# Kernel optimization log

Hardware: AMD Instinct MI355X
Metric: run time of the kernel (lower is better)

The kernel has to match this reference:

```python
import jax, jax.numpy as jnp
import numpy as np

KS = 3          # kernel_size
DIL = 6         # dilation
PAD = 6         # padding
N = KS * KS     # sampling points per pixel
EPS = 1e-5      # BatchNorm eps


def conv2d(x, w, b=None, padding=0):
    out = jax.lax.conv_general_dilated(
        x, w, window_strides=(1, 1),
        padding=[(padding, padding), (padding, padding)],
        dimension_numbers=('NCHW', 'OIHW', 'NCHW'))
    if b is not None:
        out = out + b[None, :, None, None]
    return out


def setup_inputs() -> dict:
    key = jax.random.key(0)
    ks = jax.random.split(key, 6)
    B, C, H, W, P = 4, 256, 64, 64, 256
    x = jax.random.normal(ks[0], (B, C, H, W), jnp.float32)
    # offset-predicting conv (2N channels), kaiming-ish scale, kept small so offsets are sane
    w_p = jax.random.normal(ks[1], (2 * N, C, 3, 3), jnp.float32) * 0.02
    b_p = jnp.zeros((2 * N,), jnp.float32)
    # modulation-mask conv (N channels)
    w_m = jax.random.normal(ks[2], (N, C, 3, 3), jnp.float32) * 0.02
    b_m = jnp.zeros((N,), jnp.float32)
    # main deform-conv weight (no bias)
    w = jax.random.normal(ks[3], (P, C, KS, KS), jnp.float32) * (2.0 / (C * N)) ** 0.5
    gamma = jnp.ones((P,), jnp.float32)   # BN weight (init fill 1)
    beta = jnp.zeros((P,), jnp.float32)   # BN bias  (init fill 0)
    return dict(x=x, w_p=w_p, b_p=b_p, w_m=w_m, b_m=b_m, w=w, gamma=gamma, beta=beta)


def deform_conv(x, w_p, b_p, w_m, b_m, w):
    B, C, H, W = x.shape
    offset = conv2d(x, w_p, b_p, padding=1)                 # [B, 2N, H, W]
    m = jax.nn.sigmoid(conv2d(x, w_m, b_m, padding=1))      # [B, N, H, W] modulation mask

    x_pad = jnp.pad(x, ((0, 0), (0, 0), (PAD, PAD), (PAD, PAD)))
    Hp, Wp = H + 2 * PAD, W + 2 * PAD

    # p = p_0 (base grid, starts at 1 into padded map) + p_n (dilated kernel grid) + offset
    r = (KS - 1) // 2
    pn = jnp.arange(-r, r + 1, dtype=jnp.float32) * DIL
    pn_x, pn_y = jnp.meshgrid(pn, pn, indexing='ij')        # row-major matches conv weight layout
    p0_x = jnp.arange(1, H + 1, dtype=jnp.float32)
    p0_y = jnp.arange(1, W + 1, dtype=jnp.float32)
    off_x = offset[:, :N].transpose(0, 2, 3, 1)             # [B, H, W, N]
    off_y = offset[:, N:].transpose(0, 2, 3, 1)
    px = p0_x[None, :, None, None] + pn_x.reshape(-1)[None, None, None, :] + off_x
    py = p0_y[None, None, :, None] + pn_y.reshape(-1)[None, None, None, :] + off_y

    q_lt_x = jnp.clip(jnp.floor(px), 0, Hp - 1)
    q_lt_y = jnp.clip(jnp.floor(py), 0, Wp - 1)
    q_rb_x = jnp.clip(jnp.floor(px) + 1, 0, Hp - 1)
    q_rb_y = jnp.clip(jnp.floor(py) + 1, 0, Wp - 1)
    px = jnp.clip(px, 0, Hp - 1)
    py = jnp.clip(py, 0, Wp - 1)

    x_flat = x_pad.reshape(B, C, Hp * Wp)

    def gather(qx, qy):
        idx = (qx * Wp + qy).astype(jnp.int32).reshape(B, 1, -1)   # [B,1,H*W*N]
        v = jnp.take_along_axis(x_flat, jnp.broadcast_to(idx, (B, C, idx.shape[-1])), axis=2)
        return v.reshape(B, C, H, W, N)

    # bilinear weights (deform-conv-v2 formulation)
    g_lt = (1 + (q_lt_x - px)) * (1 + (q_lt_y - py))
    g_rb = (1 - (q_rb_x - px)) * (1 - (q_rb_y - py))
    g_lb = (1 + (q_lt_x - px)) * (1 - (q_rb_y - py))
    g_rt = (1 - (q_rb_x - px)) * (1 + (q_lt_y - py))

    x_off = (g_lt[:, None] * gather(q_lt_x, q_lt_y)
             + g_rb[:, None] * gather(q_rb_x, q_rb_y)
             + g_lb[:, None] * gather(q_lt_x, q_rb_y)
             + g_rt[:, None] * gather(q_rb_x, q_lt_y))     # [B, C, H, W, N]

    x_off = x_off * m.transpose(0, 2, 3, 1)[:, None]        # apply modulation

    # stride-KS conv over the tiled x_offset == einsum over kernel positions
    wk = w.reshape(w.shape[0], C, N)
    return jnp.einsum('bchwk,ock->bohw', x_off, wk)


def reference(x, w_p, b_p, w_m, b_m, w, gamma, beta):
    y = deform_conv(x, w_p, b_p, w_m, b_m, w)
    # BatchNorm2d, training mode (batch stats, biased variance)
    mean = y.mean(axis=(0, 2, 3), keepdims=True)
    var = ((y - mean) ** 2).mean(axis=(0, 2, 3), keepdims=True)
    y = (y - mean) * jax.lax.rsqrt(var + EPS)
    y = y * gamma[None, :, None, None] + beta[None, :, None, None]
    return jax.nn.relu(y)
```

## Files before the change

### kernel.cpp

```cpp
#include <hip/hip_runtime.h>
#include <math.h>

#define CC 256
#define PP 256
#define XSTR 296

#define WS_OFF   0ull
#define WS_Y     442368ull
#define WS_SUM   4636672ull
#define WS_SUMSQ 4636928ull
#define WS_SCALE 4637184ull
#define WS_SHIFT 4637440ull
#define WS_XT    4637696ull
#define WS_WF    8832000ull
#define WS_WPMF  9126912ull

typedef __attribute__((ext_vector_type(8))) short bf16x8;
typedef __attribute__((ext_vector_type(4))) float f32x4;

static __device__ inline unsigned short f2bf(float f) {
  unsigned int u = __float_as_uint(f);
  unsigned int r = (u + 0x7FFFu + ((u >> 16) & 1u)) >> 16;
  return (unsigned short)r;
}

__global__ __launch_bounds__(256) void k_prep(const float* __restrict__ x,
                                              const float* __restrict__ w,
                                              const float* __restrict__ w_p,
                                              const float* __restrict__ w_m,
                                              float* __restrict__ ws) {
  int blk = blockIdx.x, t = threadIdx.x;
  if (blk < 1024) {
    __shared__ float sT[64][65];
    int b = blk >> 8, h = (blk >> 2) & 63, c0 = (blk & 3) * 64;
    const float* xs = x + ((size_t)(b * 256 + c0) * 64 + h) * 64;
    int cl = t >> 6, wl = t & 63;
#pragma unroll
    for (int it = 0; it < 16; ++it) {
      int c = cl + it * 4;
      sT[c][wl] = xs[(size_t)c * 4096 + wl];
    }
    __syncthreads();
    float* xt = ws + WS_XT + ((size_t)b * 64 + h) * 16384 + c0;
    int c2 = t & 63, w2l = t >> 6;
#pragma unroll
    for (int it = 0; it < 16; ++it) {
      int w2 = w2l + it * 4;
      xt[(size_t)w2 * 256 + c2] = sT[c2][w2];
    }
  } else {
    int gid = (blk - 1024) * 256 + t;
    if (blk == 1024 && t < 512) ws[WS_SUM + t] = 0.f;
    unsigned short* wfb = (unsigned short*)(ws + WS_WF);
    for (int e = gid; e < 589824; e += 163840) {
      int j = e & 7, ocin = (e >> 3) & 15, quad = (e >> 7) & 3;
      int ot = (e >> 9) & 15, ksg = e >> 13;
      int kb = ksg / 9, ks = ksg - kb * 9;
      int c = kb * 32 + quad * 8 + j;
      int oc = ot * 16 + ocin;
      wfb[e] = f2bf(w[((size_t)oc * CC + c) * 9 + ks]);
    }
    unsigned short* wpmf = (unsigned short*)(ws + WS_WPMF);
    for (int e = gid; e < 73728; e += 163840) {
      int j = e & 7, ocin = (e >> 3) & 15, quad = (e >> 7) & 3;
      int ot = (e >> 9) & 1, ksg = e >> 10;
      int kb = ksg / 9, ks = ksg - kb * 9;
      int c = kb * 32 + quad * 8 + j;
      int oc = ot * 16 + ocin;
      float v = 0.f;
      if (oc < 18)      v = w_p[((size_t)oc * CC + c) * 9 + ks];
      else if (oc < 27) v = w_m[((size_t)(oc - 18) * CC + c) * 9 + ks];
      wpmf[e] = f2bf(v);
    }
  }
}

__global__ __launch_bounds__(512, 4) void k_offmask(const float* __restrict__ b_p,
                                                    const float* __restrict__ b_m,
                                                    float* __restrict__ ws) {
  const float* xT = ws + WS_XT;
  const unsigned short* wpmf = (const unsigned short*)(ws + WS_WPMF);
  float* offm = ws + WS_OFF;
  __shared__ __align__(16) unsigned short sXo0[32 * XSTR];
  __shared__ __align__(16) unsigned short sXo1[32 * XSTR];

  int t = threadIdx.x, blk = blockIdx.x;
  int xcd = blk & 7, ii = blk >> 3;
  int b = xcd >> 1, h = (xcd & 1) * 32 + (ii >> 1), side = ii & 1;

  int lane = t & 63, wv = __builtin_amdgcn_readfirstlane(t >> 6);
  int pxt = wv & 1, ot = (wv >> 1) & 1, kh = wv >> 2;
  f32x4 acc = {0.f, 0.f, 0.f, 0.f};
  const float4* xb4 = (const float4*)(xT + (size_t)b * 1048576);
  int uq = t >> 3, q = t & 7;

  int oa[5], odst[5];
#pragma unroll
  for (int r = 0; r < 5; ++r) {
    int u = r * 64 + uq;
    if (u < 288) {
      int j = u >> 5, px = u & 31;
      int row = h + j / 3 - 1, col = side * 32 + px + j % 3 - 1;
      odst[r] = px * XSTR + j * 32 + q * 4;
      oa[r] = ((unsigned)row < 64u && (unsigned)col < 64u)
                  ? (row * 64 + col) * 64 + q : -1;
    } else {
      odst[r] = -1;
      oa[r] = -1;
    }
  }

  auto stage = [&](int kb, unsigned short* buf) {
    int cb = kb * 8;
#pragma unroll
    for (int r = 0; r < 5; ++r) {
      if (odst[r] >= 0) {
        float4 v = {0.f, 0.f, 0.f, 0.f};
        if (oa[r] >= 0) v = xb4[oa[r] + cb];
        unsigned p0 = (unsigned)f2bf(v.x) | ((unsigned)f2bf(v.y) << 16);
        unsigned p1 = (unsigned)f2bf(v.z) | ((unsigned)f2bf(v.w) << 16);
        *(uint2*)&buf[odst[r]] = (uint2){p0, p1};
      }
    }
  };

  stage(0, sXo0);
  __syncthreads();
  for (int kb = 0; kb < 8; ++kb) {
    unsigned short* cur = (kb & 1) ? sXo1 : sXo0;
    unsigned short* nxt = (kb & 1) ? sXo0 : sXo1;
    if (kb < 7) stage(kb + 1, nxt);
    const unsigned short* bb =
        &cur[(pxt * 16 + (lane & 15)) * XSTR + (lane >> 4) * 8];
#pragma unroll
    for (int ks = 0; ks < 9; ++ks) {
      if ((int)(ks >= 5) == kh) {
        int ksg = kb * 9 + ks;
        bf16x8 af =
            *(const bf16x8*)(wpmf + (size_t)ksg * 1024 + ot * 512 + lane * 8);
        bf16x8 bf = *(const bf16x8*)(bb + ks * 32);
        acc = __builtin_amdgcn_mfma_f32_16x16x32_bf16(af, bf, acc, 0, 0, 0);
      }
    }
    __syncthreads();
  }

  float* sR = (float*)sXo0;
  if (kh == 1) {
    int base = (pxt * 2 + ot) * 256 + lane * 4;
#pragma unroll
    for (int r = 0; r < 4; ++r) sR[base + r] = acc[r];
  }
  __syncthreads();
  if (kh == 0) {
    int base = (pxt * 2 + ot) * 256 + lane * 4;
    int pxl = side * 32 + pxt * 16 + (lane & 15);
#pragma unroll
    for (int r = 0; r < 4; ++r) {
      int oc = ot * 16 + (lane >> 4) * 4 + r;
      if (oc < 27) {
        float v = acc[r] + sR[base + r];
        v += (oc < 18) ? b_p[oc] : b_m[oc - 18];
        if (oc >= 18) v = 1.f / (1.f + expf(-v));
        offm[((size_t)b * 27 + oc) * 4096 + h * 64 + pxl] = v;
      }
    }
  }
}

__global__ __launch_bounds__(512, 4) void k_deform(float* __restrict__ ws) {
  const float* offm = ws + WS_OFF;
  const float* xT = ws + WS_XT;
  const unsigned short* wfb = (const unsigned short*)(ws + WS_WF);
  float* y = ws + WS_Y;

  __shared__ __align__(16) uint4 sPK[288];
  __shared__ __align__(16) unsigned short sXu0[32 * XSTR];
  __shared__ __align__(16) unsigned short sXu1[32 * XSTR];

  int t = threadIdx.x, blk = blockIdx.x;
  int xcd = blk & 7, ii = blk >> 3;
  int b = xcd >> 1, h = (xcd & 1) * 32 + (ii >> 1), side = ii & 1;

  if (t < 288) {
    int k = t >> 5, w = side * 32 + (t & 31);
    size_t base = ((size_t)b * 27) * 4096 + h * 64 + w;
    float offx = offm[base + (size_t)k * 4096];
    float offy = offm[base + (size_t)(9 + k) * 4096];
    float mk   = offm[base + (size_t)(18 + k) * 4096];
    float pnx = (float)((k / 3 - 1) * 6);
    float pny = (float)((k % 3 - 1) * 6);
    float pxf = (float)(h + 1) + pnx + offx;
    float pyf = (float)(w + 1) + pny + offy;
    float fx = floorf(pxf), fy = floorf(pyf);
    float q0x = fminf(fmaxf(fx, 0.f), 75.f);
    float q1x = fminf(fmaxf(fx + 1.f, 0.f), 75.f);
    float q0y = fminf(fmaxf(fy, 0.f), 75.f);
    float q1y = fminf(fmaxf(fy + 1.f, 0.f), 75.f);
    float pxc = fminf(fmaxf(pxf, 0.f), 75.f);
    float pyc = fminf(fmaxf(pyf, 0.f), 75.f);
    float glt = (1.f + (q0x - pxc)) * (1.f + (q0y - pyc));
    float grb = (1.f - (q1x - pxc)) * (1.f - (q1y - pyc));
    float glb = (1.f + (q0x - pxc)) * (1.f - (q1y - pyc));
    float grt = (1.f - (q1x - pxc)) * (1.f + (q0y - pyc));
    int ix0 = (int)q0x - 6, ix1 = (int)q1x - 6;
    int iy0 = (int)q0y - 6, iy1 = (int)q1y - 6;
    bool v00 = (unsigned)ix0 < 64u && (unsigned)iy0 < 64u;
    bool v11 = (unsigned)ix1 < 64u && (unsigned)iy1 < 64u;
    bool v01 = (unsigned)ix0 < 64u && (unsigned)iy1 < 64u;
    bool v10 = (unsigned)ix1 < 64u && (unsigned)iy0 < 64u;
    unsigned a0 = v00 ? (unsigned)(ix0 * 64 + iy0) : 0u;
    unsigned a1 = v11 ? (unsigned)(ix1 * 64 + iy1) : 0u;
    unsigned a2 = v01 ? (unsigned)(ix0 * 64 + iy1) : 0u;
    unsigned a3 = v10 ? (unsigned)(ix1 * 64 + iy0) : 0u;
    float g0 = v00 ? glt * mk : 0.f;
    float g1 = v11 ? grb * mk : 0.f;
    float g2 = v01 ? glb * mk : 0.f;
    float g3 = v10 ? grt * mk : 0.f;
    uint4 pk;
    pk.x = a0 | (a1 << 16);
    pk.y = a2 | (a3 << 16);
    pk.z = (unsigned)f2bf(g0) | ((unsigned)f2bf(g1) << 16);
    pk.w = (unsigned)f2bf(g2) | ((unsigned)f2bf(g3) << 16);
    sPK[t] = pk;
  }
  __syncthreads();

  int uq = t >> 3, q = t & 7;
  int ta0[5], ta1[5], ta2[5], ta3[5], tdst[5];
  float tg0[5], tg1[5], tg2[5], tg3[5];
#pragma unroll
  for (int r = 0; r < 5; ++r) {
    int u = r * 64 + uq;
    if (u < 288) {
      uint4 pk = sPK[u];
      int k = u >> 5, px = u & 31;
      ta0[r] = (int)(pk.x & 0xFFFFu) * 64 + q;
      ta1[r] = (int)(pk.x >> 16) * 64 + q;
      ta2[r] = (int)(pk.y & 0xFFFFu) * 64 + q;
      ta3[r] = (int)(pk.y >> 16) * 64 + q;
      tg0[r] = __uint_as_float((pk.z & 0xFFFFu) << 16);
      tg1[r] = __uint_as_float(pk.z & 0xFFFF0000u);
      tg2[r] = __uint_as_float((pk.w & 0xFFFFu) << 16);
      tg3[r] = __uint_as_float(pk.w & 0xFFFF0000u);
      tdst[r] = px * XSTR + k * 32 + q * 4;
    } else {
      tdst[r] = -1;
    }
  }

  int lane = t & 63, wv = __builtin_amdgcn_readfirstlane(t >> 6);
  f32x4 acc[2][2];
#pragma unroll
  for (int i = 0; i < 2; ++i)
#pragma unroll
    for (int jj = 0; jj < 2; ++jj) acc[i][jj] = (f32x4){0.f, 0.f, 0.f, 0.f};

  const float4* xb4 = (const float4*)(xT + (size_t)b * 1048576);

  auto stage = [&](int kb, unsigned short* buf) {
    int cb = kb * 8;
#pragma unroll
    for (int r = 0; r < 5; ++r) {
      if (tdst[r] >= 0) {
        float4 v0 = xb4[ta0[r] + cb];
        float4 v1 = xb4[ta1[r] + cb];
        float4 v2 = xb4[ta2[r] + cb];
        float4 v3 = xb4[ta3[r] + cb];
        float g0 = tg0[r], g1 = tg1[r], g2 = tg2[r], g3 = tg3[r];
        float4 val;
        val.x = fmaf(g3, v3.x, fmaf(g2, v2.x, fmaf(g1, v1.x, g0 * v0.x)));
        val.y = fmaf(g3, v3.y, fmaf(g2, v2.y, fmaf(g1, v1.y, g0 * v0.y)));
        val.z = fmaf(g3, v3.z, fmaf(g2, v2.z, fmaf(g1, v1.z, g0 * v0.z)));
        val.w = fmaf(g3, v3.w, fmaf(g2, v2.w, fmaf(g1, v1.w, g0 * v0.w)));
        unsigned p0 = (unsigned)f2bf(val.x) | ((unsigned)f2bf(val.y) << 16);
        unsigned p1 = (unsigned)f2bf(val.z) | ((unsigned)f2bf(val.w) << 16);
        *(uint2*)&buf[tdst[r]] = (uint2){p0, p1};
      }
    }
  };

  stage(0, sXu0);
  __syncthreads();
  for (int kb = 0; kb < 8; ++kb) {
    unsigned short* cur = (kb & 1) ? sXu1 : sXu0;
    unsigned short* nxt = (kb & 1) ? sXu0 : sXu1;
    if (kb < 7) stage(kb + 1, nxt);
    const unsigned short* bb0 = &cur[(lane & 15) * XSTR + (lane >> 4) * 8];
    const unsigned short* bb1 = bb0 + 16 * XSTR;
#pragma unroll
    for (int ks = 0; ks < 9; ++ks) {
      int ksg = kb * 9 + ks;
      const unsigned short* ap =
          wfb + (size_t)ksg * 8192 + (size_t)wv * 1024 + lane * 8;
      bf16x8 af0 = *(const bf16x8*)ap;
      bf16x8 af1 = *(const bf16x8*)(ap + 512);
      bf16x8 bf0 = *(const bf16x8*)(bb0 + ks * 32);
      bf16x8 bf1 = *(const bf16x8*)(bb1 + ks * 32);
      acc[0][0] = __builtin_amdgcn_mfma_f32_16x16x32_bf16(af0, bf0, acc[0][0], 0, 0, 0);
      acc[0][1] = __builtin_amdgcn_mfma_f32_16x16x32_bf16(af0, bf1, acc[0][1], 0, 0, 0);
      acc[1][0] = __builtin_amdgcn_mfma_f32_16x16x32_bf16(af1, bf0, acc[1][0], 0, 0, 0);
      acc[1][1] = __builtin_amdgcn_mfma_f32_16x16x32_bf16(af1, bf1, acc[1][1], 0, 0, 0);
    }
    __syncthreads();
  }

  float* sP = (float*)sPK;
  float* sP2 = sP + 256;
  int quad = lane >> 4, li = lane & 15;
  size_t ybase = ((size_t)b * PP) * 4096 + h * 64 + side * 32;
#pragma unroll
  for (int otl = 0; otl < 2; ++otl) {
#pragma unroll
    for (int r = 0; r < 4; ++r) {
      int oc = wv * 32 + otl * 16 + quad * 4 + r;
      float v0 = acc[otl][0][r];
      float v1 = acc[otl][1][r];
      float* yp = y + ybase + (size_t)oc * 4096 + li;
      yp[0] = v0;
      yp[16] = v1;
      float s = v0 + v1;
      float s2 = fmaf(v0, v0, v1 * v1);
      s += __shfl_xor(s, 1);  s2 += __shfl_xor(s2, 1);
      s += __shfl_xor(s, 2);  s2 += __shfl_xor(s2, 2);
      s += __shfl_xor(s, 4);  s2 += __shfl_xor(s2, 4);
      s += __shfl_xor(s, 8);  s2 += __shfl_xor(s2, 8);
      if (li == 0) {
        sP[oc] = s;
        sP2[oc] = s2;
      }
    }
  }
  __syncthreads();
  if (t < 256) {
    atomicAdd(&ws[WS_SUM + t], sP[t]);
    atomicAdd(&ws[WS_SUMSQ + t], sP2[t]);
  }
}

__global__ void k_stats(float* __restrict__ ws, const float* __restrict__ gamma,
                        const float* __restrict__ beta) {
  int t = threadIdx.x;
  float s  = ws[WS_SUM + t];
  float s2 = ws[WS_SUMSQ + t];
  float mean = s * (1.f / 16384.f);
  float var  = fmaf(s2, 1.f / 16384.f, -mean * mean);
  float rstd = rsqrtf(var + 1e-5f);
  float sc = gamma[t] * rstd;
  ws[WS_SCALE + t] = sc;
  ws[WS_SHIFT + t] = fmaf(-mean, sc, beta[t]);
}

__global__ void k_bnrelu(const float* __restrict__ ws, float* __restrict__ out) {
  const float4* y4 = (const float4*)(ws + WS_Y);
  const float* scale = ws + WS_SCALE;
  const float* shift = ws + WS_SHIFT;
  float4* o4 = (float4*)out;
  const int n4 = 4 * PP * 1024;
  for (int i = blockIdx.x * blockDim.x + threadIdx.x; i < n4;
       i += gridDim.x * blockDim.x) {
    int oc = (i >> 10) & 255;
    float sc = scale[oc], sh = shift[oc];
    float4 v = y4[i];
    float4 r;
    r.x = fmaxf(fmaf(v.x, sc, sh), 0.f);
    r.y = fmaxf(fmaf(v.y, sc, sh), 0.f);
    r.z = fmaxf(fmaf(v.z, sc, sh), 0.f);
    r.w = fmaxf(fmaf(v.w, sc, sh), 0.f);
    o4[i] = r;
  }
}

extern "C" void kernel_launch(void* const* d_in, const int* in_sizes, int n_in,
                              void* d_out, int out_size, void* d_ws,
                              size_t ws_size, hipStream_t stream) {
  const float* x     = (const float*)d_in[0];
  const float* w_p   = (const float*)d_in[1];
  const float* b_p   = (const float*)d_in[2];
  const float* w_m   = (const float*)d_in[3];
  const float* b_m   = (const float*)d_in[4];
  const float* w     = (const float*)d_in[5];
  const float* gamma = (const float*)d_in[6];
  const float* beta  = (const float*)d_in[7];
  float* ws  = (float*)d_ws;
  float* out = (float*)d_out;

  k_prep<<<1664, 256, 0, stream>>>(x, w, w_p, w_m, ws);
  k_offmask<<<512, 512, 0, stream>>>(b_p, b_m, ws);
  k_deform<<<512, 512, 0, stream>>>(ws);
  k_stats<<<1, 256, 0, stream>>>(ws, gamma, beta);
  k_bnrelu<<<2048, 256, 0, stream>>>(ws, out);
}
```

Baseline: 167.9 us.

## Store transposed input as bf16 and gather 8-channel vectors in deform/offset kernels

The prep kernel now writes the channel-last copy of x as bf16 instead of fp32, halving the workspace footprint and the gather traffic in both the offset/mask conv and the deformable sampling kernel. Each thread now loads 16-byte bf16x8 vectors covering 8 channels, and the thread-to-sample mapping changes from 8 to 4 threads per sample. The deform kernel drops the shared-memory packing stage and its barrier, so each thread computes its own bilinear addresses and weights redundantly. The scratch for the epilogue reuses a staging buffer. The cost is that input values are rounded to bf16 before bilinear interpolation rather than after, which adds an extra rounding step.

```diff
diff --git a/kernel.cpp b/kernel.cpp
--- a/kernel.cpp
+++ b/kernel.cpp
@@ -12,8 +12,8 @@
 #define WS_SCALE 4637184ull
 #define WS_SHIFT 4637440ull
 #define WS_XT    4637696ull
-#define WS_WF    8832000ull
-#define WS_WPMF  9126912ull
+#define WS_WF    6734848ull
+#define WS_WPMF  7029760ull
 
 typedef __attribute__((ext_vector_type(8))) short bf16x8;
 typedef __attribute__((ext_vector_type(4))) float f32x4;
@@ -22,6 +22,9 @@
   unsigned int u = __float_as_uint(f);
   unsigned int r = (u + 0x7FFFu + ((u >> 16) & 1u)) >> 16;
   return (unsigned short)r;
+}
+static __device__ inline float bf2f(short s) {
+  return __uint_as_float(((unsigned)(unsigned short)s) << 16);
 }
 
 __global__ __launch_bounds__(256) void k_prep(const float* __restrict__ x,
@@ -41,12 +44,13 @@
       sT[c][wl] = xs[(size_t)c * 4096 + wl];
     }
     __syncthreads();
-    float* xt = ws + WS_XT + ((size_t)b * 64 + h) * 16384 + c0;
+    unsigned short* xt = (unsigned short*)(ws + WS_XT) +
+                         ((size_t)b * 64 + h) * 16384 + c0;
     int c2 = t & 63, w2l = t >> 6;
 #pragma unroll
     for (int it = 0; it < 16; ++it) {
       int w2 = w2l + it * 4;
-      xt[(size_t)w2 * 256 + c2] = sT[c2][w2];
+      xt[(size_t)w2 * 256 + c2] = f2bf(sT[c2][w2]);
     }
   } else {
     int gid = (blk - 1024) * 256 + t;
@@ -78,7 +82,7 @@
 __global__ __launch_bounds__(512, 4) void k_offmask(const float* __restrict__ b_p,
                                                     const float* __restrict__ b_m,
                                                     float* __restrict__ ws) {
-  const float* xT = ws + WS_XT;
+  const unsigned short* xT = (const unsigned short*)(ws + WS_XT);
   const unsigned short* wpmf = (const unsigned short*)(ws + WS_WPMF);
   float* offm = ws + WS_OFF;
   __shared__ __align__(16) unsigned short sXo0[32 * XSTR];
@@ -91,35 +95,32 @@
   int lane = t & 63, wv = __builtin_amdgcn_readfirstlane(t >> 6);
   int pxt = wv & 1, ot = (wv >> 1) & 1, kh = wv >> 2;
   f32x4 acc = {0.f, 0.f, 0.f, 0.f};
-  const float4* xb4 = (const float4*)(xT + (size_t)b * 1048576);
-  int uq = t >> 3, q = t & 7;
-
-  int oa[5], odst[5];
-#pragma unroll
-  for (int r = 0; r < 5; ++r) {
-    int u = r * 64 + uq;
+  const unsigned short* xb = xT + (size_t)b * 1048576;
+  int q = t & 3, uq = t >> 2;
+
+  int oa[3], odst[3];
+#pragma unroll
+  for (int r = 0; r < 3; ++r) {
+    int u = r * 128 + uq;
+    odst[r] = -1;
+    oa[r] = -1;
     if (u < 288) {
       int j = u >> 5, px = u & 31;
       int row = h + j / 3 - 1, col = side * 32 + px + j % 3 - 1;
-      odst[r] = px * XSTR + j * 32 + q * 4;
-      oa[r] = ((unsigned)row < 64u && (unsigned)col < 64u)
-                  ? (row * 64 + col) * 64 + q : -1;
-    } else {
-      odst[r] = -1;
-      oa[r] = -1;
+      odst[r] = px * XSTR + j * 32 + q * 8;
+      if ((unsigned)row < 64u && (unsigned)col < 64u)
+        oa[r] = (row * 64 + col) * 256 + q * 8;
     }
   }
 
   auto stage = [&](int kb, unsigned short* buf) {
-    int cb = kb * 8;
-#pragma unroll
-    for (int r = 0; r < 5; ++r) {
+    int cb = kb * 32;
+#pragma unroll
+    for (int r = 0; r < 3; ++r) {
       if (odst[r] >= 0) {
-        float4 v = {0.f, 0.f, 0.f, 0.f};
-        if (oa[r] >= 0) v = xb4[oa[r] + cb];
-        unsigned p0 = (unsigned)f2bf(v.x) | ((unsigned)f2bf(v.y) << 16);
-        unsigned p1 = (unsigned)f2bf(v.z) | ((unsigned)f2bf(v.w) << 16);
-        *(uint2*)&buf[odst[r]] = (uint2){p0, p1};
+        bf16x8 v = {0, 0, 0, 0, 0, 0, 0, 0};
+        if (oa[r] >= 0) v = *(const bf16x8*)(xb + oa[r] + cb);
+        *(bf16x8*)&buf[odst[r]] = v;
       }
     }
   };
@@ -170,11 +171,10 @@
 
 __global__ __launch_bounds__(512, 4) void k_deform(float* __restrict__ ws) {
   const float* offm = ws + WS_OFF;
-  const float* xT = ws + WS_XT;
+  const unsigned short* xT = (const unsigned short*)(ws + WS_XT);
   const unsigned short* wfb = (const unsigned short*)(ws + WS_WF);
   float* y = ws + WS_Y;
 
-  __shared__ __align__(16) uint4 sPK[288];
   __shared__ __align__(16) unsigned short sXu0[32 * XSTR];
   __shared__ __align__(16) unsigned short sXu1[32 * XSTR];
 
@@ -182,70 +182,50 @@
   int xcd = blk & 7, ii = blk >> 3;
   int b = xcd >> 1, h = (xcd & 1) * 32 + (ii >> 1), side = ii & 1;
 
-  if (t < 288) {
-    int k = t >> 5, w = side * 32 + (t & 31);
-    size_t base = ((size_t)b * 27) * 4096 + h * 64 + w;
-    float offx = offm[base + (size_t)k * 4096];
-    float offy = offm[base + (size_t)(9 + k) * 4096];
-    float mk   = offm[base + (size_t)(18 + k) * 4096];
-    float pnx = (float)((k / 3 - 1) * 6);
-    float pny = (float)((k % 3 - 1) * 6);
-    float pxf = (float)(h + 1) + pnx + offx;
-    float pyf = (float)(w + 1) + pny + offy;
-    float fx = floorf(pxf), fy = floorf(pyf);
-    float q0x = fminf(fmaxf(fx, 0.f), 75.f);
-    float q1x = fminf(fmaxf(fx + 1.f, 0.f), 75.f);
-    float q0y = fminf(fmaxf(fy, 0.f), 75.f);
-    float q1y = fminf(fmaxf(fy + 1.f, 0.f), 75.f);
-    float pxc = fminf(fmaxf(pxf, 0.f), 75.f);
-    float pyc = fminf(fmaxf(pyf, 0.f), 75.f);
-    float glt = (1.f + (q0x - pxc)) * (1.f + (q0y - pyc));
-    float grb = (1.f - (q1x - pxc)) * (1.f - (q1y - pyc));
-    float glb = (1.f + (q0x - pxc)) * (1.f - (q1y - pyc));
-    float grt = (1.f - (q1x - pxc)) * (1.f + (q0y - pyc));
-    int ix0 = (int)q0x - 6, ix1 = (int)q1x - 6;
-    int iy0 = (int)q0y - 6, iy1 = (int)q1y - 6;
-    bool v00 = (unsigned)ix0 < 64u && (unsigned)iy0 < 64u;
-    bool v11 = (unsigned)ix1 < 64u && (unsigned)iy1 < 64u;
-    bool v01 = (unsigned)ix0 < 64u && (unsigned)iy1 < 64u;
-    bool v10 = (unsigned)ix1 < 64u && (unsigned)iy0 < 64u;
-    unsigned a0 = v00 ? (unsigned)(ix0 * 64 + iy0) : 0u;
-    unsigned a1 = v11 ? (unsigned)(ix1 * 64 + iy1) : 0u;
-    unsigned a2 = v01 ? (unsigned)(ix0 * 64 + iy1) : 0u;
-    unsigned a3 = v10 ? (unsigned)(ix1 * 64 + iy0) : 0u;
-    float g0 = v00 ? glt * mk : 0.f;
-    float g1 = v11 ? grb * mk : 0.f;
-    float g2 = v01 ? glb * mk : 0.f;
-    float g3 = v10 ? grt * mk : 0.f;
-    uint4 pk;
-    pk.x = a0 | (a1 << 16);
-    pk.y = a2 | (a3 << 16);
-    pk.z = (unsigned)f2bf(g0) | ((unsigned)f2bf(g1) << 16);
-    pk.w = (unsigned)f2bf(g2) | ((unsigned)f2bf(g3) << 16);
-    sPK[t] = pk;
-  }
-  __syncthreads();
-
-  int uq = t >> 3, q = t & 7;
-  int ta0[5], ta1[5], ta2[5], ta3[5], tdst[5];
-  float tg0[5], tg1[5], tg2[5], tg3[5];
-#pragma unroll
-  for (int r = 0; r < 5; ++r) {
-    int u = r * 64 + uq;
+  int q = t & 3, uq = t >> 2;
+  int ta0[3], ta1[3], ta2[3], ta3[3], tdst[3];
+  float tg0[3], tg1[3], tg2[3], tg3[3];
+#pragma unroll
+  for (int r = 0; r < 3; ++r) {
+    int u = r * 128 + uq;
+    tdst[r] = -1;
     if (u < 288) {
-      uint4 pk = sPK[u];
       int k = u >> 5, px = u & 31;
-      ta0[r] = (int)(pk.x & 0xFFFFu) * 64 + q;
-      ta1[r] = (int)(pk.x >> 16) * 64 + q;
-      ta2[r] = (int)(pk.y & 0xFFFFu) * 64 + q;
-      ta3[r] = (int)(pk.y >> 16) * 64 + q;
-      tg0[r] = __uint_as_float((pk.z & 0xFFFFu) << 16);
-      tg1[r] = __uint_as_float(pk.z & 0xFFFF0000u);
-      tg2[r] = __uint_as_float((pk.w & 0xFFFFu) << 16);
-      tg3[r] = __uint_as_float(pk.w & 0xFFFF0000u);
-      tdst[r] = px * XSTR + k * 32 + q * 4;
-    } else {
-      tdst[r] = -1;
+      int w = side * 32 + px;
+      size_t base = ((size_t)b * 27) * 4096 + h * 64 + w;
+      float offx = offm[base + (size_t)k * 4096];
+      float offy = offm[base + (size_t)(9 + k) * 4096];
+      float mk   = offm[base + (size_t)(18 + k) * 4096];
+      float pnx = (float)((k / 3 - 1) * 6);
+      float pny = (float)((k % 3 - 1) * 6);
+      float pxf = (float)(h + 1) + pnx + offx;
+      float pyf = (float)(w + 1) + pny + offy;
+      float fx = floorf(pxf), fy = floorf(pyf);
+      float q0x = fminf(fmaxf(fx, 0.f), 75.f);
+      float q1x = fminf(fmaxf(fx + 1.f, 0.f), 75.f);
+      float q0y = fminf(fmaxf(fy, 0.f), 75.f);
+      float q1y = fminf(fmaxf(fy + 1.f, 0.f), 75.f);
+      float pxc = fminf(fmaxf(pxf, 0.f), 75.f);
+      float pyc = fminf(fmaxf(pyf, 0.f), 75.f);
+      float glt = (1.f + (q0x - pxc)) * (1.f + (q0y - pyc));
+      float grb = (1.f - (q1x - pxc)) * (1.f - (q1y - pyc));
+      float glb = (1.f + (q0x - pxc)) * (1.f - (q1y - pyc));
+      float grt = (1.f - (q1x - pxc)) * (1.f + (q0y - pyc));
+      int ix0 = (int)q0x - 6, ix1 = (int)q1x - 6;
+      int iy0 = (int)q0y - 6, iy1 = (int)q1y - 6;
+      bool v00 = (unsigned)ix0 < 64u && (unsigned)iy0 < 64u;
+      bool v11 = (unsigned)ix1 < 64u && (unsigned)iy1 < 64u;
+      bool v01 = (unsigned)ix0 < 64u && (unsigned)iy1 < 64u;
+      bool v10 = (unsigned)ix1 < 64u && (unsigned)iy0 < 64u;
+      ta0[r] = (v00 ? (ix0 * 64 + iy0) : 0) * 256 + q * 8;
+      ta1[r] = (v11 ? (ix1 * 64 + iy1) : 0) * 256 + q * 8;
+      ta2[r] = (v01 ? (ix0 * 64 + iy1) : 0) * 256 + q * 8;
+      ta3[r] = (v10 ? (ix1 * 64 + iy0) : 0) * 256 + q * 8;
+      tg0[r] = v00 ? glt * mk : 0.f;
+      tg1[r] = v11 ? grb * mk : 0.f;
+      tg2[r] = v01 ? glb * mk : 0.f;
+      tg3[r] = v10 ? grt * mk : 0.f;
+      tdst[r] = px * XSTR + k * 32 + q * 8;
     }
   }
 
@@ -256,26 +236,33 @@
 #pragma unroll
     for (int jj = 0; jj < 2; ++jj) acc[i][jj] = (f32x4){0.f, 0.f, 0.f, 0.f};
 
-  const float4* xb4 = (const float4*)(xT + (size_t)b * 1048576);
+  const unsigned short* xb = xT + (size_t)b * 1048576;
 
   auto stage = [&](int kb, unsigned short* buf) {
-    int cb = kb * 8;
-#pragma unroll
-    for (int r = 0; r < 5; ++r) {
+    int cb = kb * 32;
+#pragma unroll
+    for (int r = 0; r < 3; ++r) {
       if (tdst[r] >= 0) {
-        float4 v0 = xb4[ta0[r] + cb];
-        float4 v1 = xb4[ta1[r] + cb];
-        float4 v2 = xb4[ta2[r] + cb];
-        float4 v3 = xb4[ta3[r] + cb];
+        bf16x8 t0 = *(const bf16x8*)(xb + ta0[r] + cb);
+        bf16x8 t1 = *(const bf16x8*)(xb + ta1[r] + cb);
+        bf16x8 t2 = *(const bf16x8*)(xb + ta2[r] + cb);
+        bf16x8 t3 = *(const bf16x8*)(xb + ta3[r] + cb);
         float g0 = tg0[r], g1 = tg1[r], g2 = tg2[r], g3 = tg3[r];
-        float4 val;
-        val.x = fmaf(g3, v3.x, fmaf(g2, v2.x, fmaf(g1, v1.x, g0 * v0.x)));
-        val.y = fmaf(g3, v3.y, fmaf(g2, v2.y, fmaf(g1, v1.y, g0 * v0.y)));
-        val.z = fmaf(g3, v3.z, fmaf(g2, v2.z, fmaf(g1, v1.z, g0 * v0.z)));
-        val.w = fmaf(g3, v3.w, fmaf(g2, v2.w, fmaf(g1, v1.w, g0 * v0.w)));
-        unsigned p0 = (unsigned)f2bf(val.x) | ((unsigned)f2bf(val.y) << 16);
-        unsigned p1 = (unsigned)f2bf(val.z) | ((unsigned)f2bf(val.w) << 16);
-        *(uint2*)&buf[tdst[r]] = (uint2){p0, p1};
+        unsigned short pk[8];
+#pragma unroll
+        for (int i = 0; i < 8; ++i) {
+          float val = g0 * bf2f(t0[i]);
+          val = fmaf(g1, bf2f(t1[i]), val);
+          val = fmaf(g2, bf2f(t2[i]), val);
+          val = fmaf(g3, bf2f(t3[i]), val);
+          pk[i] = f2bf(val);
+        }
+        uint4 w4;
+        w4.x = (unsigned)pk[0] | ((unsigned)pk[1] << 16);
+        w4.y = (unsigned)pk[2] | ((unsigned)pk[3] << 16);
+        w4.z = (unsigned)pk[4] | ((unsigned)pk[5] << 16);
+        w4.w = (unsigned)pk[6] | ((unsigned)pk[7] << 16);
+        *(uint4*)&buf[tdst[r]] = w4;
       }
     }
   };
@@ -305,7 +292,7 @@
     __syncthreads();
   }
 
-  float* sP = (float*)sPK;
+  float* sP = (float*)sXu0;
   float* sP2 = sP + 256;
   int quad = lane >> 4, li = lane & 15;
   size_t ybase = ((size_t)b * PP) * 4096 + h * 64 + side * 32;
```

Result: faster. 159.0 us (-5.3%).
